# Optimization experiments

Measured on AMD Instinct MI355X. Metric: run time of the kernel, lower is better.

## Reference

```python
import jax, jax.numpy as jnp
import numpy as np

_INF = -1e+30
N_HEAD, D_MODEL, D_HEAD = 16, 1024, 64
SCALE = 1.0 / float(np.sqrt(D_HEAD))
LN_EPS = 1e-5


def layer_norm(x, g, b):
    mu = jnp.mean(x, axis=-1, keepdims=True)
    var = jnp.mean(jnp.square(x - mu), axis=-1, keepdims=True)
    return (x - mu) * jax.lax.rsqrt(var + LN_EPS) * g + b


def setup_inputs() -> dict:
    key = jax.random.key(0)
    k_h, k_m, k_q, k_k, k_v, k_o = jax.random.split(key, 6)
    B, S = 2, 2048
    h = jax.random.normal(k_h, (B, S, D_MODEL), dtype=jnp.float32)
    attn_mask = jax.random.randint(k_m, (B, S), 0, 2, dtype=jnp.int32)
    # torch Linear weights: [out_features, in_features], init N(0, scale)
    q_w = jax.random.normal(k_q, (N_HEAD * D_HEAD, D_MODEL), dtype=jnp.float32) * SCALE
    k_w = jax.random.normal(k_k, (N_HEAD * D_HEAD, D_MODEL), dtype=jnp.float32) * SCALE
    v_w = jax.random.normal(k_v, (N_HEAD * D_HEAD, D_MODEL), dtype=jnp.float32) * SCALE
    o_w = jax.random.normal(k_o, (D_MODEL, N_HEAD * D_HEAD), dtype=jnp.float32) * SCALE
    ln_g = jnp.ones((D_MODEL,), dtype=jnp.float32)
    ln_b = jnp.zeros((D_MODEL,), dtype=jnp.float32)
    return {"h": h, "attn_mask": attn_mask, "q_w": q_w, "k_w": k_w,
            "v_w": v_w, "o_w": o_w, "ln_g": ln_g, "ln_b": ln_b}


def reference(h, attn_mask, q_w, k_w, v_w, o_w, ln_g, ln_b):
    B, S, _ = h.shape
    # mems=None -> c == h; pre_lnorm=False
    head_q = (h @ q_w.T).reshape(B, S, N_HEAD, D_HEAD)
    head_k = (h @ k_w.T).reshape(B, S, N_HEAD, D_HEAD)
    head_v = (h @ v_w.T).reshape(B, S, N_HEAD, D_HEAD)
    # scores [b, i(q), j(k), n]
    attn_score = jnp.einsum('bind,bjnd->bijn', head_q, head_k) * SCALE
    mask = (attn_mask == 0)[:, None, :, None]  # [b,1,j,1]
    attn_score = jnp.where(mask, _INF, attn_score)
    attn_prob = jax.nn.softmax(attn_score, axis=2)
    attn_vec = jnp.einsum('bijn,bjnd->bind', attn_prob, head_v)
    attn_vec = attn_vec.reshape(B, S, N_HEAD * D_HEAD)
    attn_out = attn_vec @ o_w.T
    output = h + attn_out  # dropout=0 -> identity
    return layer_norm(output, ln_g, ln_b)  # post-lnorm
```

## Files before the change

### kernel.cpp

```cpp
#include <hip/hip_runtime.h>
#include <hip/hip_bf16.h>

typedef __attribute__((ext_vector_type(8))) _Float16 hfx8;
typedef __attribute__((ext_vector_type(16))) float fx16;
typedef __attribute__((ext_vector_type(2))) __fp16 fp16x2;
typedef __attribute__((ext_vector_type(4))) float fx4;
typedef __attribute__((ext_vector_type(4))) unsigned short usx4;
typedef __attribute__((ext_vector_type(8))) unsigned short usx8;
typedef __attribute__((ext_vector_type(2))) unsigned int ux2;

#define LOG2E 1.44269504f

__device__ __forceinline__ unsigned short f2h(float f) {
  union { _Float16 h; unsigned short u; } c;
  c.h = (_Float16)f;
  return c.u;
}

__device__ __forceinline__ void async16(const void* g, void* l) {
  __builtin_amdgcn_global_load_lds(
      (const __attribute__((address_space(1))) void*)g,
      (__attribute__((address_space(3))) void*)l, 16, 0, 0);
}

__global__ __launch_bounds__(256)
void cvth(const float* __restrict__ s, unsigned short* __restrict__ d) {
  int i = (blockIdx.x * 256 + threadIdx.x) * 4;
  fx4 v = *(const fx4*)(s + i);
  usx4 o;
  o[0] = f2h(v[0]); o[1] = f2h(v[1]); o[2] = f2h(v[2]); o[3] = f2h(v[3]);
  *(usx4*)(d + i) = o;
}

__global__ __launch_bounds__(256)
void cvtw(const float* __restrict__ s0, const float* __restrict__ s1,
          const float* __restrict__ s2, const float* __restrict__ s3,
          unsigned short* __restrict__ d0, unsigned short* __restrict__ d1,
          unsigned short* __restrict__ d2, unsigned short* __restrict__ d3) {
  const int y = blockIdx.y;
  const float* s = (y == 0) ? s0 : (y == 1) ? s1 : (y == 2) ? s2 : s3;
  unsigned short* d = (y == 0) ? d0 : (y == 1) ? d1 : (y == 2) ? d2 : d3;
  int i = (blockIdx.x * 256 + threadIdx.x) * 4;
  fx4 v = *(const fx4*)(s + i);
  usx4 o;
  o[0] = f2h(v[0]); o[1] = f2h(v[1]); o[2] = f2h(v[2]); o[3] = f2h(v[3]);
  *(usx4*)(d + i) = o;
}

__global__ __launch_bounds__(256)
void maskscan(const int* __restrict__ mask, int* __restrict__ perm, int* __restrict__ cnt) {
  const int b = blockIdx.x;
  const int tid = threadIdx.x;
  const int base = b * 2048 + tid * 8;
  int m[8];
  int s = 0;
#pragma unroll
  for (int e = 0; e < 8; ++e) { m[e] = mask[base + e] ? 1 : 0; s += m[e]; }
  const int lane = tid & 63, wv = tid >> 6;
  int inc = s;
#pragma unroll
  for (int off = 1; off < 64; off <<= 1) {
    int t = __shfl_up(inc, off);
    if (lane >= off) inc += t;
  }
  __shared__ int wsum[4];
  if (lane == 63) wsum[wv] = inc;
  __syncthreads();
  int wvoff = 0;
#pragma unroll
  for (int k = 0; k < 4; ++k)
    if (k < wv) wvoff += wsum[k];
  int run = wvoff + inc - s;
#pragma unroll
  for (int e = 0; e < 8; ++e) {
    perm[base + e] = m[e] ? (b * 2048 + run) : -1;
    run += m[e];
  }
  if (tid == 255) cnt[b] = run;
}

__global__ __launch_bounds__(256, 2)
void gemm_qkv(const unsigned short* __restrict__ A,
              const unsigned short* __restrict__ Wq,
              const unsigned short* __restrict__ Wk,
              const unsigned short* __restrict__ Wv,
              const int* __restrict__ perm,
              unsigned short* __restrict__ Qf, unsigned short* __restrict__ Kf,
              unsigned short* __restrict__ Vt) {
  __shared__ unsigned short As[2][128 * 64];
  __shared__ unsigned short Bs[2][128 * 64];
  const int tid = threadIdx.x;
  const int w = tid >> 6, ln = tid & 63;
  const int mt = blockIdx.x;
  const int by = blockIdx.y;
  const int sel = by >> 3;
  const int nt = by & 7;
  const unsigned short* W = (sel == 0) ? Wq : ((sel == 1) ? Wk : Wv);
  const int m0 = mt * 128, n0 = nt * 128;
  const int wr = w >> 1, wc = w & 1;
  fx4 acc[4][4] = {};

  const int lr = ln >> 3;
  const int scg = (ln & 7) ^ lr;
  const unsigned short* Asrc = A + (size_t)(m0 + w * 32 + lr) * 1024 + scg * 8;
  const unsigned short* Bsrc = W + (size_t)(n0 + w * 32 + lr) * 1024 + scg * 8;

#define G_STAGE(KT, BI)                                                        \
  {                                                                            \
    _Pragma("unroll") for (int i = 0; i < 4; ++i) {                            \
      async16(Asrc + (size_t)i * 8 * 1024 + (KT) * 64, &As[BI][(w * 32 + i * 8) * 64]); \
      async16(Bsrc + (size_t)i * 8 * 1024 + (KT) * 64, &Bs[BI][(w * 32 + i * 8) * 64]); \
    }                                                                          \
  }

  G_STAGE(0, 0);
  for (int kt = 0; kt < 16; ++kt) {
    const int cur = kt & 1;
    __syncthreads();
    if (kt < 15) G_STAGE(kt + 1, cur ^ 1);
#pragma unroll
    for (int kk = 0; kk < 2; ++kk) {
      const int kg = kk * 4 + (ln >> 4);
      hfx8 af[4], bfr[4];
#pragma unroll
      for (int mi = 0; mi < 4; ++mi) {
        int row = wr * 64 + mi * 16 + (ln & 15);
        af[mi] = *(const hfx8*)&As[cur][row * 64 + ((kg ^ (row & 7)) * 8)];
      }
#pragma unroll
      for (int ni = 0; ni < 4; ++ni) {
        int row = wc * 64 + ni * 16 + (ln & 15);
        bfr[ni] = *(const hfx8*)&Bs[cur][row * 64 + ((kg ^ (row & 7)) * 8)];
      }
#pragma unroll
      for (int mi = 0; mi < 4; ++mi)
#pragma unroll
        for (int ni = 0; ni < 4; ++ni)
          acc[mi][ni] = __builtin_amdgcn_mfma_f32_16x16x32_f16(af[mi], bfr[ni], acc[mi][ni], 0, 0, 0);
    }
  }
#undef G_STAGE
  const int cb = n0 + wc * 64 + (ln & 15);
  const int rb = m0 + wr * 64 + ((ln >> 4) << 2);
  if (sel == 0) {
#pragma unroll
    for (int mi = 0; mi < 4; ++mi)
#pragma unroll
      for (int ni = 0; ni < 4; ++ni)
#pragma unroll
        for (int j = 0; j < 4; ++j)
          Qf[(size_t)(rb + mi * 16 + j) * 1024 + cb + ni * 16] = f2h(acc[mi][ni][j] * 0.125f);
  } else if (sel == 1) {
#pragma unroll
    for (int mi = 0; mi < 4; ++mi)
#pragma unroll
      for (int ni = 0; ni < 4; ++ni)
#pragma unroll
        for (int j = 0; j < 4; ++j) {
          int r = rb + mi * 16 + j;
          int pv = perm[r];
          if (pv >= 0)
            Kf[(size_t)pv * 1024 + cb + ni * 16] = f2h(acc[mi][ni][j]);
        }
  } else {
#pragma unroll
    for (int mi = 0; mi < 4; ++mi)
#pragma unroll
      for (int ni = 0; ni < 4; ++ni) {
        int c = cb + ni * 16;
        int hh = (c >> 6) & 15, dd = c & 63;
#pragma unroll
        for (int j = 0; j < 4; ++j) {
          int r = rb + mi * 16 + j;
          int pv = perm[r];
          if (pv >= 0) {
            int bI = r >> 11;
            int sc = pv & 2047;
            Vt[((size_t)(bI * 16 + hh) * 64 + dd) * 2048 + sc] = f2h(acc[mi][ni][j]);
          }
        }
      }
  }
}

__global__ __launch_bounds__(256, 2)
void gemm_o(const unsigned short* __restrict__ A,
            const unsigned short* __restrict__ W,
            float* __restrict__ O) {
  __shared__ unsigned short As[2][128 * 64];
  __shared__ unsigned short Bs[2][128 * 64];
  const int tid = threadIdx.x;
  const int w = tid >> 6, ln = tid & 63;
  const int mt = blockIdx.x, nt = blockIdx.y;
  const int m0 = mt * 128, n0 = nt * 128;
  const int wr = w >> 1, wc = w & 1;
  fx4 acc[4][4] = {};
  const int lr = ln >> 3;
  const int scg = (ln & 7) ^ lr;
  const unsigned short* Asrc = A + (size_t)(m0 + w * 32 + lr) * 1024 + scg * 8;
  const unsigned short* Bsrc = W + (size_t)(n0 + w * 32 + lr) * 1024 + scg * 8;

#define G_STAGE(KT, BI)                                                        \
  {                                                                            \
    _Pragma("unroll") for (int i = 0; i < 4; ++i) {                            \
      async16(Asrc + (size_t)i * 8 * 1024 + (KT) * 64, &As[BI][(w * 32 + i * 8) * 64]); \
      async16(Bsrc + (size_t)i * 8 * 1024 + (KT) * 64, &Bs[BI][(w * 32 + i * 8) * 64]); \
    }                                                                          \
  }

  G_STAGE(0, 0);
  for (int kt = 0; kt < 16; ++kt) {
    const int cur = kt & 1;
    __syncthreads();
    if (kt < 15) G_STAGE(kt + 1, cur ^ 1);
#pragma unroll
    for (int kk = 0; kk < 2; ++kk) {
      const int kg = kk * 4 + (ln >> 4);
      hfx8 af[4], bfr[4];
#pragma unroll
      for (int mi = 0; mi < 4; ++mi) {
        int row = wr * 64 + mi * 16 + (ln & 15);
        af[mi] = *(const hfx8*)&As[cur][row * 64 + ((kg ^ (row & 7)) * 8)];
      }
#pragma unroll
      for (int ni = 0; ni < 4; ++ni) {
        int row = wc * 64 + ni * 16 + (ln & 15);
        bfr[ni] = *(const hfx8*)&Bs[cur][row * 64 + ((kg ^ (row & 7)) * 8)];
      }
#pragma unroll
      for (int mi = 0; mi < 4; ++mi)
#pragma unroll
        for (int ni = 0; ni < 4; ++ni)
          acc[mi][ni] = __builtin_amdgcn_mfma_f32_16x16x32_f16(af[mi], bfr[ni], acc[mi][ni], 0, 0, 0);
    }
  }
#undef G_STAGE
  const int cb = n0 + wc * 64 + (ln & 15);
  const int rb = m0 + wr * 64 + ((ln >> 4) << 2);
#pragma unroll
  for (int mi = 0; mi < 4; ++mi)
#pragma unroll
    for (int ni = 0; ni < 4; ++ni)
#pragma unroll
      for (int j = 0; j < 4; ++j)
        O[(size_t)(rb + mi * 16 + j) * 1024 + cb + ni * 16] = acc[mi][ni][j];
}

__global__ __launch_bounds__(256, 2)
void attn_fwd(const unsigned short* __restrict__ Qf,
              const unsigned short* __restrict__ Kf,
              const unsigned short* __restrict__ Vt,
              const int* __restrict__ cnt,
              unsigned short* __restrict__ Ov) {
  __shared__ __align__(16) unsigned short smem[32768];
  unsigned short (*Ks)[8192] = (unsigned short (*)[8192])(smem);
  unsigned short (*Vs)[8192] = (unsigned short (*)[8192])(smem + 16384);
  unsigned short* eb = smem;

  const int tid = threadIdx.x;
  const int w = tid >> 6, ln = tid & 63;
  const int qt = blockIdx.x, h = blockIdx.y, b = blockIdx.z;
  const int l31 = ln & 31, h5 = ln >> 5;
  const int q = qt * 128 + w * 32 + l31;

  const int cnt_b = cnt[b];
  const int ntile = (cnt_b + 127) >> 7;

  hfx8 qb[4];
  {
    const unsigned short* qp = Qf + (size_t)(b * 2048 + q) * 1024 + h * 64 + h5 * 8;
    qb[0] = *(const hfx8*)(qp);
    qb[1] = *(const hfx8*)(qp + 16);
    qb[2] = *(const hfx8*)(qp + 32);
    qb[3] = *(const hfx8*)(qp + 48);
  }

  fx16 o0 = {}, o1 = {};
  float mrow = -INFINITY, lrow = 0.f;

#define A_STAGE(KT, BI)                                                          \
  {                                                                              \
    _Pragma("unroll") for (int ii = 0; ii < 4; ++ii) {                           \
      int krow = w * 32 + ii * 8 + (ln >> 3);                                    \
      async16(Kf + ((size_t)(b * 2048 + (KT) * 128 + krow)) * 1024 + h * 64 +    \
                  (((ln & 7) ^ (ln >> 3)) * 8),                                  \
              &Ks[BI][(w * 4 + ii) * 512]);                                      \
      int vswz = (ii * 4 + (ln >> 4)) & 7;                                       \
      int vrow = w * 16 + ii * 4 + (ln >> 4);                                    \
      async16(Vt + ((size_t)((b * 16 + h) * 64 + vrow)) * 2048 + (KT) * 128 +    \
                  (((ln & 15) ^ vswz) * 8),                                      \
              &Vs[BI][(w * 4 + ii) * 512]);                                      \
    }                                                                            \
  }

  A_STAGE(0, 0);
  for (int kt = 0; kt < ntile; ++kt) {
    const int cur = kt & 1;
    __syncthreads();
    if (kt + 1 < ntile) A_STAGE(kt + 1, cur ^ 1);
    const bool lastt = (kt == ntile - 1);

    fx16 sArr[4];
#pragma unroll
    for (int kb = 0; kb < 4; ++kb) {
      fx16 z = {};
      if (lastt) {
#pragma unroll
        for (int r = 0; r < 16; ++r) {
          int crow = (r & 3) + 8 * (r >> 2) + 4 * h5;
          int key = kt * 128 + kb * 32 + crow;
          z[r] = (key < cnt_b) ? 0.0f : -1e30f;
        }
      }
#pragma unroll
      for (int dc = 0; dc < 4; ++dc) {
        int row = kb * 32 + l31;
        int slot = (dc * 2 + h5) ^ (l31 & 7);
        hfx8 a = *(const hfx8*)&Ks[cur][row * 64 + slot * 8];
        z = __builtin_amdgcn_mfma_f32_32x32x16_f16(a, qb[dc], z, 0, 0, 0);
      }
      sArr[kb] = z;
    }

    float tm = -INFINITY;
#pragma unroll
    for (int kb = 0; kb < 4; ++kb)
#pragma unroll
      for (int r = 0; r < 16; ++r) tm = fmaxf(tm, sArr[kb][r]);
    tm = fmaxf(tm, __shfl_xor(tm, 32));
    if (!__all(tm <= mrow + 8.0f)) {
      float mn = fmaxf(mrow, tm);
      float fac = exp2f((mrow - mn) * LOG2E);
      mrow = mn;
      lrow *= fac;
#pragma unroll
      for (int r = 0; r < 16; ++r) { o0[r] *= fac; o1[r] *= fac; }
    }
    const float nm2 = -mrow * LOG2E;
    float psum = 0.f;
    unsigned int pk[4][8];
#pragma unroll
    for (int kb = 0; kb < 4; ++kb) {
#pragma unroll
      for (int j = 0; j < 8; ++j) {
        float pa = exp2f(fmaf(sArr[kb][2 * j], LOG2E, nm2));
        float pb = exp2f(fmaf(sArr[kb][2 * j + 1], LOG2E, nm2));
        psum += pa + pb;
        union { fp16x2 h; unsigned int u; } rr;
        rr.h = __builtin_amdgcn_cvt_pkrtz(pa, pb);
        pk[kb][j] = rr.u;
      }
    }
    psum += __shfl_xor(psum, 32);
    lrow += psum;

#pragma unroll
    for (int kc = 0; kc < 8; ++kc) {
      const int kbq = kc >> 1;
      const int jb = (kc & 1) * 4;
      unsigned int s00 = pk[kbq][jb],     s01 = pk[kbq][jb + 1];
      unsigned int s10 = pk[kbq][jb + 2], s11 = pk[kbq][jb + 3];
      unsigned int keep0 = h5 ? s10 : s00, keep1 = h5 ? s11 : s01;
      unsigned int send0 = h5 ? s00 : s10, send1 = h5 ? s01 : s11;
      unsigned int rec0 = (unsigned int)__shfl_xor((int)send0, 32);
      unsigned int rec1 = (unsigned int)__shfl_xor((int)send1, 32);
      union { unsigned int u[4]; hfx8 v; } B_;
      B_.u[0] = h5 ? rec0 : keep0;
      B_.u[1] = h5 ? rec1 : keep1;
      B_.u[2] = h5 ? keep0 : rec0;
      B_.u[3] = h5 ? keep1 : rec1;
      int slot = (kc * 2 + h5) ^ (l31 & 7);
      hfx8 va0 = *(const hfx8*)&Vs[cur][(l31) * 128 + slot * 8];
      o0 = __builtin_amdgcn_mfma_f32_32x32x16_f16(va0, B_.v, o0, 0, 0, 0);
      hfx8 va1 = *(const hfx8*)&Vs[cur][(32 + l31) * 128 + slot * 8];
      o1 = __builtin_amdgcn_mfma_f32_32x32x16_f16(va1, B_.v, o1, 0, 0, 0);
    }
  }
#undef A_STAGE

  __syncthreads();
  float inv = 1.0f / lrow;
  const int ql = w * 32 + l31;
#pragma unroll
  for (int db = 0; db < 2; ++db) {
#pragma unroll
    for (int r4 = 0; r4 < 4; ++r4) {
      float v0 = (db ? o1[4 * r4] : o0[4 * r4]) * inv;
      float v1 = (db ? o1[4 * r4 + 1] : o0[4 * r4 + 1]) * inv;
      float v2 = (db ? o1[4 * r4 + 2] : o0[4 * r4 + 2]) * inv;
      float v3 = (db ? o1[4 * r4 + 3] : o0[4 * r4 + 3]) * inv;
      union { fp16x2 h; unsigned int u; } pa_, pb_;
      pa_.h = __builtin_amdgcn_cvt_pkrtz(v0, v1);
      pb_.h = __builtin_amdgcn_cvt_pkrtz(v2, v3);
      ux2 tw; tw[0] = pa_.u; tw[1] = pb_.u;
      int d_base = db * 32 + 8 * r4 + 4 * h5;
      *(ux2*)&eb[ql * 88 + d_base] = tw;
    }
  }
  __syncthreads();
#pragma unroll
  for (int pass = 0; pass < 4; ++pass) {
    int idx = pass * 256 + tid;
    int qq = idx >> 3, slot = idx & 7;
    usx8 vv = *(const usx8*)&eb[qq * 88 + slot * 8];
    *(usx8*)&Ov[(size_t)(b * 2048 + qt * 128 + qq) * 1024 + h * 64 + slot * 8] = vv;
  }
}

__global__ __launch_bounds__(256)
void lnk(const float* __restrict__ h, const float* __restrict__ ao,
         const float* __restrict__ g, const float* __restrict__ bb,
         float* __restrict__ out) {
  const int row = blockIdx.x;
  const int tid = threadIdx.x;
  const size_t base = (size_t)row * 1024 + tid * 4;
  fx4 x = *(const fx4*)(h + base);
  fx4 a = *(const fx4*)(ao + base);
  x = x + a;
  float s = x[0] + x[1] + x[2] + x[3];
  float q = x[0] * x[0] + x[1] * x[1] + x[2] * x[2] + x[3] * x[3];
#pragma unroll
  for (int mm = 1; mm < 64; mm <<= 1) {
    s += __shfl_xor(s, mm);
    q += __shfl_xor(q, mm);
  }
  __shared__ float rs[4], rq[4];
  if ((tid & 63) == 0) { rs[tid >> 6] = s; rq[tid >> 6] = q; }
  __syncthreads();
  s = rs[0] + rs[1] + rs[2] + rs[3];
  q = rq[0] + rq[1] + rq[2] + rq[3];
  float mu = s * (1.0f / 1024.0f);
  float var = q * (1.0f / 1024.0f) - mu * mu;
  float rstd = rsqrtf(var + 1e-5f);
  fx4 gg = *(const fx4*)(g + tid * 4);
  fx4 bv = *(const fx4*)(bb + tid * 4);
  fx4 ov;
#pragma unroll
  for (int k = 0; k < 4; ++k) ov[k] = (x[k] - mu) * rstd * gg[k] + bv[k];
  *(fx4*)(out + base) = ov;
}

extern "C" void kernel_launch(void* const* d_in, const int* in_sizes, int n_in,
                              void* d_out, int out_size, void* d_ws, size_t ws_size,
                              hipStream_t stream) {
  const float* h = (const float*)d_in[0];
  const int* msk = (const int*)d_in[1];
  const float* qw = (const float*)d_in[2];
  const float* kw = (const float*)d_in[3];
  const float* vw = (const float*)d_in[4];
  const float* ow = (const float*)d_in[5];
  const float* lng = (const float*)d_in[6];
  const float* lnb = (const float*)d_in[7];
  float* out = (float*)d_out;
  char* ws = (char*)d_ws;

  const size_t MB = 1u << 20;
  unsigned short* h16 = (unsigned short*)(ws + 0 * MB);
  unsigned short* w16q = (unsigned short*)(ws + 8 * MB);
  unsigned short* w16k = (unsigned short*)(ws + 10 * MB);
  unsigned short* w16v = (unsigned short*)(ws + 12 * MB);
  unsigned short* w16o = (unsigned short*)(ws + 14 * MB);
  unsigned short* Qf  = (unsigned short*)(ws + 16 * MB);
  unsigned short* Kf  = (unsigned short*)(ws + 24 * MB);
  unsigned short* Vtb = (unsigned short*)(ws + 32 * MB);
  unsigned short* Av  = (unsigned short*)(ws + 40 * MB);
  float* Ao = (float*)(ws + 48 * MB);
  int* perm = (int*)(ws + 48 * MB);
  int* cnt  = (int*)(ws + 48 * MB + 16384);

  cvth<<<dim3(4096), 256, 0, stream>>>(h, h16);
  cvtw<<<dim3(1024, 4), 256, 0, stream>>>(qw, kw, vw, ow, w16q, w16k, w16v, w16o);
  maskscan<<<dim3(2), 256, 0, stream>>>(msk, perm, cnt);

  gemm_qkv<<<dim3(32, 24), 256, 0, stream>>>(h16, w16q, w16k, w16v, perm, Qf, Kf, Vtb);
  attn_fwd<<<dim3(16, 16, 2), 256, 0, stream>>>(Qf, Kf, Vtb, cnt, Av);
  gemm_o<<<dim3(32, 8), 256, 0, stream>>>(Av, w16o, Ao);
  lnk<<<dim3(4096), 256, 0, stream>>>(h, Ao, lng, lnb, out);
}
```

Before: 129.7 us.

## Gather unmasked rows before K/V projection and skip fully masked tiles

The mask scan now writes a compacted list of source row indices instead of a scatter permutation. The K and V projections gather only the unmasked rows of h, so tiles beyond the valid count exit early. This removes roughly half of the K/V GEMM work and the per-element scattered stores. V transposed stores become packed vector writes. Padded rows clamp to the last valid row, so a few duplicate rows are computed and written beyond the count.

```diff
diff --git a/kernel.cpp b/kernel.cpp
--- a/kernel.cpp
+++ b/kernel.cpp
@@ -48,7 +48,7 @@
 }
 
 __global__ __launch_bounds__(256)
-void maskscan(const int* __restrict__ mask, int* __restrict__ perm, int* __restrict__ cnt) {
+void maskscan(const int* __restrict__ mask, int* __restrict__ src, int* __restrict__ cnt) {
   const int b = blockIdx.x;
   const int tid = threadIdx.x;
   const int base = b * 2048 + tid * 8;
@@ -73,8 +73,7 @@
   int run = wvoff + inc - s;
 #pragma unroll
   for (int e = 0; e < 8; ++e) {
-    perm[base + e] = m[e] ? (b * 2048 + run) : -1;
-    run += m[e];
+    if (m[e]) { src[b * 2048 + run] = tid * 8 + e; ++run; }
   }
   if (tid == 255) cnt[b] = run;
 }
@@ -84,7 +83,7 @@
               const unsigned short* __restrict__ Wq,
               const unsigned short* __restrict__ Wk,
               const unsigned short* __restrict__ Wv,
-              const int* __restrict__ perm,
+              const int* __restrict__ src, const int* __restrict__ cnt,
               unsigned short* __restrict__ Qf, unsigned short* __restrict__ Kf,
               unsigned short* __restrict__ Vt) {
   __shared__ unsigned short As[2][128 * 64];
@@ -96,20 +95,40 @@
   const int sel = by >> 3;
   const int nt = by & 7;
   const unsigned short* W = (sel == 0) ? Wq : ((sel == 1) ? Wk : Wv);
-  const int m0 = mt * 128, n0 = nt * 128;
+  const int n0 = nt * 128;
   const int wr = w >> 1, wc = w & 1;
-  fx4 acc[4][4] = {};
 
   const int lr = ln >> 3;
   const int scg = (ln & 7) ^ lr;
-  const unsigned short* Asrc = A + (size_t)(m0 + w * 32 + lr) * 1024 + scg * 8;
+
+  const int bI = mt >> 4;
+  const int r0 = (mt & 15) * 128;
+  int cnt_b = 0;
+  const unsigned short* Arow[4];
+  if (sel == 0) {
+    const int m0 = mt * 128;
+#pragma unroll
+    for (int ii = 0; ii < 4; ++ii)
+      Arow[ii] = A + (size_t)(m0 + w * 32 + ii * 8 + lr) * 1024 + scg * 8;
+  } else {
+    cnt_b = cnt[bI];
+    if (r0 >= cnt_b) return;
+#pragma unroll
+    for (int ii = 0; ii < 4; ++ii) {
+      int r = r0 + w * 32 + ii * 8 + lr;
+      r = (r < cnt_b) ? r : (cnt_b - 1);
+      Arow[ii] = A + (size_t)(bI * 2048 + src[bI * 2048 + r]) * 1024 + scg * 8;
+    }
+  }
   const unsigned short* Bsrc = W + (size_t)(n0 + w * 32 + lr) * 1024 + scg * 8;
 
-#define G_STAGE(KT, BI)                                                        \
+  fx4 acc[4][4] = {};
+
+#define G_STAGE(KT, BI_)                                                       \
   {                                                                            \
     _Pragma("unroll") for (int i = 0; i < 4; ++i) {                            \
-      async16(Asrc + (size_t)i * 8 * 1024 + (KT) * 64, &As[BI][(w * 32 + i * 8) * 64]); \
-      async16(Bsrc + (size_t)i * 8 * 1024 + (KT) * 64, &Bs[BI][(w * 32 + i * 8) * 64]); \
+      async16(Arow[i] + (KT) * 64, &As[BI_][(w * 32 + i * 8) * 64]);           \
+      async16(Bsrc + (size_t)i * 8 * 1024 + (KT) * 64, &Bs[BI_][(w * 32 + i * 8) * 64]); \
     }                                                                          \
   }
 
@@ -141,45 +160,38 @@
   }
 #undef G_STAGE
   const int cb = n0 + wc * 64 + (ln & 15);
-  const int rb = m0 + wr * 64 + ((ln >> 4) << 2);
+  const int rloc = wr * 64 + ((ln >> 4) << 2);
   if (sel == 0) {
+    const int m0 = mt * 128;
 #pragma unroll
     for (int mi = 0; mi < 4; ++mi)
 #pragma unroll
       for (int ni = 0; ni < 4; ++ni)
 #pragma unroll
         for (int j = 0; j < 4; ++j)
-          Qf[(size_t)(rb + mi * 16 + j) * 1024 + cb + ni * 16] = f2h(acc[mi][ni][j] * 0.125f);
+          Qf[(size_t)(m0 + rloc + mi * 16 + j) * 1024 + cb + ni * 16] = f2h(acc[mi][ni][j] * 0.125f);
   } else if (sel == 1) {
 #pragma unroll
     for (int mi = 0; mi < 4; ++mi)
 #pragma unroll
       for (int ni = 0; ni < 4; ++ni)
 #pragma unroll
-        for (int j = 0; j < 4; ++j) {
-          int r = rb + mi * 16 + j;
-          int pv = perm[r];
-          if (pv >= 0)
-            Kf[(size_t)pv * 1024 + cb + ni * 16] = f2h(acc[mi][ni][j]);
-        }
+        for (int j = 0; j < 4; ++j)
+          Kf[(size_t)(bI * 2048 + r0 + rloc + mi * 16 + j) * 1024 + cb + ni * 16] = f2h(acc[mi][ni][j]);
   } else {
+    const int hh = (cb >> 6) & 15, dd = cb & 63;
 #pragma unroll
     for (int mi = 0; mi < 4; ++mi)
 #pragma unroll
       for (int ni = 0; ni < 4; ++ni) {
         int c = cb + ni * 16;
-        int hh = (c >> 6) & 15, dd = c & 63;
-#pragma unroll
-        for (int j = 0; j < 4; ++j) {
-          int r = rb + mi * 16 + j;
-          int pv = perm[r];
-          if (pv >= 0) {
-            int bI = r >> 11;
-            int sc = pv & 2047;
-            Vt[((size_t)(bI * 16 + hh) * 64 + dd) * 2048 + sc] = f2h(acc[mi][ni][j]);
-          }
-        }
-      }
+        int h2 = (c >> 6) & 15, d2 = c & 63;
+        usx4 pk;
+#pragma unroll
+        for (int j = 0; j < 4; ++j) pk[j] = f2h(acc[mi][ni][j]);
+        *(usx4*)&Vt[((size_t)(bI * 16 + h2) * 64 + d2) * 2048 + r0 + rloc + mi * 16] = pk;
+      }
+    (void)hh; (void)dd;
   }
 }
 
@@ -465,14 +477,14 @@
   unsigned short* Vtb = (unsigned short*)(ws + 32 * MB);
   unsigned short* Av  = (unsigned short*)(ws + 40 * MB);
   float* Ao = (float*)(ws + 48 * MB);
-  int* perm = (int*)(ws + 48 * MB);
-  int* cnt  = (int*)(ws + 48 * MB + 16384);
+  int* srcIdx = (int*)(ws + 48 * MB);
+  int* cnt    = (int*)(ws + 48 * MB + 16384);
 
   cvth<<<dim3(4096), 256, 0, stream>>>(h, h16);
   cvtw<<<dim3(1024, 4), 256, 0, stream>>>(qw, kw, vw, ow, w16q, w16k, w16v, w16o);
-  maskscan<<<dim3(2), 256, 0, stream>>>(msk, perm, cnt);
-
-  gemm_qkv<<<dim3(32, 24), 256, 0, stream>>>(h16, w16q, w16k, w16v, perm, Qf, Kf, Vtb);
+  maskscan<<<dim3(2), 256, 0, stream>>>(msk, srcIdx, cnt);
+
+  gemm_qkv<<<dim3(32, 24), 256, 0, stream>>>(h16, w16q, w16k, w16v, srcIdx, cnt, Qf, Kf, Vtb);
   attn_fwd<<<dim3(16, 16, 2), 256, 0, stream>>>(Qf, Kf, Vtb, cnt, Av);
   gemm_o<<<dim3(32, 8), 256, 0, stream>>>(Av, w16o, Ao);
   lnk<<<dim3(4096), 256, 0, stream>>>(h, Ao, lng, lnb, out);
```

Result: faster. 124.7 us (-3.9%).
